# Optimization experiments

Measured on AMD Instinct MI355X. Metric: run time of the kernel, lower is better.

## Reference

```python
import jax, jax.numpy as jnp
import numpy as np

N = 20000      # nodes per snapshot
E = 160000     # edges per snapshot
T = 8          # timesteps
F_IN = 256     # nfeat
HEADS = 4      # GAT heads
C = 128        # nhid_graph (per-head GAT out, concat=False -> mean)
GH = 128       # nhid_gru
NC = 2         # nclass
NEG_SLOPE = 0.2


def setup_inputs() -> dict:
    key = jax.random.key(0)
    ks = jax.random.split(key, 16)
    s = 0.05
    return {
        "graph": jax.random.randint(ks[0], (T, 2, E), 0, N),
        "fts": jax.random.normal(ks[1], (T, N, F_IN), dtype=jnp.float32),
        "time_steps": T,
        # GATConv params (PyG-style): lin weight, att_src/att_dst, bias
        "W_gat": jax.random.normal(ks[2], (F_IN, HEADS * C), dtype=jnp.float32) * s,
        "att_src": jax.random.normal(ks[3], (HEADS, C), dtype=jnp.float32) * s,
        "att_dst": jax.random.normal(ks[4], (HEADS, C), dtype=jnp.float32) * s,
        "b_gat": jax.random.normal(ks[5], (C,), dtype=jnp.float32) * s,
        # GRU params (torch layout: [3H, in], gates order r,z,n)
        "W_ih": jax.random.normal(ks[6], (3 * GH, C), dtype=jnp.float32) * s,
        "W_hh": jax.random.normal(ks[7], (3 * GH, GH), dtype=jnp.float32) * s,
        "b_ih": jax.random.normal(ks[8], (3 * GH,), dtype=jnp.float32) * s,
        "b_hh": jax.random.normal(ks[9], (3 * GH,), dtype=jnp.float32) * s,
        # Attention ('general'): linear_in [H,H] no bias, linear_out [H,2H] no bias
        "W_att_in": jax.random.normal(ks[10], (GH, GH), dtype=jnp.float32) * s,
        "W_att_out": jax.random.normal(ks[11], (GH, 2 * GH), dtype=jnp.float32) * s,
        # final classifier
        "W_cls": jax.random.normal(ks[12], (NC, GH), dtype=jnp.float32) * s,
        "b_cls": jax.random.normal(ks[13], (NC,), dtype=jnp.float32) * s,
    }


def _segment_softmax(logits, seg, num_segments):
    # logits: [E', H], seg: [E'] destination node ids
    m = jax.ops.segment_max(logits, seg, num_segments=num_segments)
    m = jnp.where(jnp.isfinite(m), m, 0.0)
    e = jnp.exp(logits - m[seg])
    s = jax.ops.segment_sum(e, seg, num_segments=num_segments)
    return e / (s[seg] + 1e-16)


def _gat_step(x, edge_index, W_gat, att_src, att_dst, b_gat):
    # PyG GATConv: concat=False (mean over heads), negative_slope=0.2,
    # add_self_loops=True; eval mode so attention dropout is identity.
    n = x.shape[0]
    xw = (x @ W_gat).reshape(n, HEADS, C)                 # [N,H,C]
    loops = jnp.arange(n, dtype=edge_index.dtype)
    src = jnp.concatenate([edge_index[0], loops])         # [E']
    dst = jnp.concatenate([edge_index[1], loops])
    a_src = jnp.einsum('nhc,hc->nh', xw, att_src)         # [N,H]
    a_dst = jnp.einsum('nhc,hc->nh', xw, att_dst)
    alpha = jax.nn.leaky_relu(a_src[src] + a_dst[dst], NEG_SLOPE)  # [E',H]
    alpha = _segment_softmax(alpha, dst, n)
    msg = xw[src] * alpha[..., None]                      # [E',H,C]
    out = jax.ops.segment_sum(msg, dst, num_segments=n)   # [N,H,C]
    return out.mean(axis=1) + b_gat                       # [N,C]


def _gru(y, W_ih, W_hh, b_ih, b_hh):
    # y: [T, N, C]; torch GRU equations, h0 = 0
    n = y.shape[1]
    def step(h, x):
        gi = x @ W_ih.T + b_ih
        gh = h @ W_hh.T + b_hh
        i_r, i_z, i_n = jnp.split(gi, 3, axis=-1)
        h_r, h_z, h_n = jnp.split(gh, 3, axis=-1)
        r = jax.nn.sigmoid(i_r + h_r)
        z = jax.nn.sigmoid(i_z + h_z)
        nn_ = jnp.tanh(i_n + r * h_n)
        h_new = (1.0 - z) * nn_ + z * h
        return h_new, h_new
    h0 = jnp.zeros((n, GH), dtype=y.dtype)
    last, full = jax.lax.scan(step, h0, y)
    return full, last  # [T,N,GH], [N,GH]


def reference(graph, fts, time_steps, W_gat, att_src, att_dst, b_gat,
              W_ih, W_hh, b_ih, b_hh, W_att_in, W_att_out, W_cls, b_cls):
    # per-timestep GAT + leaky_relu(0.2)
    ys = [jax.nn.leaky_relu(
            _gat_step(fts[i], graph[i], W_gat, att_src, att_dst, b_gat),
            NEG_SLOPE)
          for i in range(time_steps)]
    y = jnp.stack(ys)                                     # [T,N,C]
    context, last = _gru(y, W_ih, W_hh, b_ih, b_hh)
    query = last[:, None, :]                              # [N,1,GH]
    context = jnp.transpose(context, (1, 0, 2))           # [N,T,GH]
    # Attention('general')
    q = query @ W_att_in.T                                # [N,1,GH]
    scores = jnp.einsum('nod,ntd->not', q, context)       # [N,1,T]
    w = jax.nn.softmax(scores, axis=-1)
    mix = jnp.einsum('not,ntd->nod', w, context)          # [N,1,GH]
    combined = jnp.concatenate([mix, q], axis=-1)         # [N,1,2GH]
    att_out = jnp.tanh(combined @ W_att_out.T)            # [N,1,GH]
    output = jax.nn.leaky_relu(att_out.reshape(-1, GH), NEG_SLOPE)
    logits = output @ W_cls.T + b_cls                     # [N,NC]
    return jax.nn.log_softmax(logits, axis=1)
```

## Files before the change

kernel.cpp:

```cpp
#include <hip/hip_runtime.h>
#include <hip/hip_bf16.h>
#include <math.h>

#define N_NODES 20000
#define N_EDGES 160000
#define T_STEPS 8
#define F_INC   256
#define HEADS   4
#define CCH     128
#define KC      512
#define GHD     128
#define G3      384
#define SLOPE   0.2f
#define SEG     (N_EDGES + N_NODES)

typedef unsigned short u16;
typedef __attribute__((ext_vector_type(8))) short bf16x8;
typedef __attribute__((ext_vector_type(4))) float f32x4;

__device__ __forceinline__ float leakyf(float x) { return x > 0.f ? x : SLOPE * x; }
__device__ __forceinline__ float b2f(u16 u) {
  union { unsigned int i; float f; } x; x.i = ((unsigned int)u) << 16; return x.f;
}
__device__ __forceinline__ u16 f2b(float f) {
  union { float f; unsigned int i; } u; u.f = f;
  unsigned int r = u.i + 0x7FFFu + ((u.i >> 16) & 1u);
  return (u16)(r >> 16);
}
__device__ __forceinline__ float sigf(float x) { return 1.f / (1.f + expf(-x)); }

__device__ __forceinline__ void gload16(const void* g, void* l) {
  __builtin_amdgcn_global_load_lds(
      (const __attribute__((address_space(1))) unsigned int*)g,
      (__attribute__((address_space(3))) unsigned int*)l, 16, 0, 0);
}

__device__ __forceinline__ bf16x8 cvt8(f32x4 lo, f32x4 hi) {
  union { unsigned int u[4]; bf16x8 v; } r;
  asm("v_cvt_pk_bf16_f32 %0, %1, %2" : "=v"(r.u[0]) : "v"(lo[0]), "v"(lo[1]));
  asm("v_cvt_pk_bf16_f32 %0, %1, %2" : "=v"(r.u[1]) : "v"(lo[2]), "v"(lo[3]));
  asm("v_cvt_pk_bf16_f32 %0, %1, %2" : "=v"(r.u[2]) : "v"(hi[0]), "v"(hi[1]));
  asm("v_cvt_pk_bf16_f32 %0, %1, %2" : "=v"(r.u[3]) : "v"(hi[2]), "v"(hi[3]));
  return r.v;
}

template <int OBF, int FUSE, int AFP32>
__global__ __launch_bounds__(256) void gemm_bf16(
    const void* __restrict__ Ain, const u16* __restrict__ B,
    const float* __restrict__ bias, void* __restrict__ Cout,
    int M, int K, int Nt, int swz,
    const float* __restrict__ attS, const float* __restrict__ attD,
    float* __restrict__ asrc, float* __restrict__ adst)
{
  __shared__ __align__(16) char AsRaw[128 * 32 * 4];
  __shared__ u16 Bs[128][32];
  __shared__ float s_as[128], s_ad[128];
  float* AsF = (float*)AsRaw;
  u16 (*Asb)[32] = (u16(*)[32])AsRaw;
  const int tid  = threadIdx.x;
  const int wave = tid >> 6, lane = tid & 63;
  const int wr = (wave >> 1) * 64, wc = (wave & 1) * 64;
  int bx = blockIdx.x, by = blockIdx.y;
  if (swz) {
    const int gx = gridDim.x;
    const int nwg = gx * (int)gridDim.y;
    const int lin = by * gx + bx;
    const int q = nwg >> 3, r = nwg & 7;
    const int xcd = lin & 7, idx = lin >> 3;
    const int wg = (xcd < r ? xcd * (q + 1) : r * (q + 1) + (xcd - r) * q) + idx;
    bx = wg % gx; by = wg / gx;
  }
  const int bm = by * 128, bn = bx * 128;
  const int l15 = lane & 15, g = lane >> 4;

  if (FUSE && tid < 128) { s_as[tid] = 0.f; s_ad[tid] = 0.f; }

  const int sr = tid >> 2, sd = tid & 3;
  const int ss = sd ^ ((sr >> 1) & 3);
  const u16* aS0 = 0; const u16* aS1 = 0; u16* lA0 = 0; u16* lA1 = 0;
  const float* aF[4]; float* lAF[4];
  if (AFP32) {
    const float* Af = (const float*)Ain;
    const int row0 = tid >> 3, sd8 = tid & 7;
    const int ss8 = sd8 ^ (row0 & 7);
    #pragma unroll
    for (int p = 0; p < 4; ++p) {
      int row = row0 + p * 32;
      aF[p] = Af + (size_t)min(bm + row, M - 1) * K + ss8 * 4;
      lAF[p] = AsF + (size_t)(p * 256 + (tid & ~63)) * 4;
    }
  } else {
    const u16* Ab = (const u16*)Ain;
    aS0 = Ab + (size_t)min(bm + sr,      M - 1) * K + ss * 8;
    aS1 = Ab + (size_t)min(bm + 64 + sr, M - 1) * K + ss * 8;
    lA0 = (u16*)AsRaw + (size_t)(tid & ~63) * 8;
    lA1 = lA0 + 2048;
  }
  const u16* bS0 = B + (size_t)(bn + sr)      * K + ss * 8;
  const u16* bS1 = B + (size_t)(bn + 64 + sr) * K + ss * 8;
  u16* lB0 = &Bs[0][0] + (size_t)(tid & ~63) * 8;
  u16* lB1 = lB0 + 2048;

  f32x4 acc[4][4];
  #pragma unroll
  for (int m = 0; m < 4; ++m)
    #pragma unroll
    for (int n = 0; n < 4; ++n)
      #pragma unroll
      for (int j = 0; j < 4; ++j) acc[m][n][j] = 0.f;

  const int nK = K >> 5;
  for (int kt = 0; kt < nK; ++kt) {
    const int ko = kt * 32;
    if (AFP32) {
      #pragma unroll
      for (int p = 0; p < 4; ++p) gload16(aF[p] + ko, lAF[p]);
    } else {
      gload16(aS0 + ko, lA0);
      gload16(aS1 + ko, lA1);
    }
    gload16(bS0 + ko, lB0);
    gload16(bS1 + ko, lB1);
    __syncthreads();
    bf16x8 af[4], bfr[4];
    #pragma unroll
    for (int m = 0; m < 4; ++m) {
      int row = wr + m * 16 + l15;
      if (AFP32) {
        int s0 = (2 * g) ^ (row & 7), s1 = (2 * g + 1) ^ (row & 7);
        f32x4 lo = *(const f32x4*)&AsF[row * 32 + s0 * 4];
        f32x4 hi = *(const f32x4*)&AsF[row * 32 + s1 * 4];
        af[m] = cvt8(lo, hi);
      } else {
        af[m] = *(const bf16x8*)&Asb[row][(g ^ ((row >> 1) & 3)) * 8];
      }
      int rowb = wc + m * 16 + l15;
      bfr[m] = *(const bf16x8*)&Bs[rowb][(g ^ ((rowb >> 1) & 3)) * 8];
    }
    #pragma unroll
    for (int m = 0; m < 4; ++m)
      #pragma unroll
      for (int n = 0; n < 4; ++n)
        acc[m][n] = __builtin_amdgcn_mfma_f32_16x16x32_bf16(af[m], bfr[n], acc[m][n], 0, 0, 0);
    __syncthreads();
  }
  #pragma unroll
  for (int m = 0; m < 4; ++m) {
    int row0 = bm + wr + m * 16 + g * 4;
    #pragma unroll
    for (int n = 0; n < 4; ++n) {
      int col = bn + wc + n * 16 + l15;
      float bv = bias ? bias[col] : 0.f;
      #pragma unroll
      for (int j = 0; j < 4; ++j) {
        int row = row0 + j;
        if (row < M) {
          float v = acc[m][n][j] + bv;
          if (OBF) ((u16*)Cout)[(size_t)row * Nt + col] = f2b(v);
          else     ((float*)Cout)[(size_t)row * Nt + col] = v;
        }
      }
    }
  }
  if (FUSE) {
    float ps[4][4], pd[4][4];
    #pragma unroll
    for (int m = 0; m < 4; ++m)
      #pragma unroll
      for (int j = 0; j < 4; ++j) { ps[m][j] = 0.f; pd[m][j] = 0.f; }
    #pragma unroll
    for (int n = 0; n < 4; ++n) {
      int cl = wc + n * 16 + l15;
      float wsv = attS[bn + cl], wdv = attD[bn + cl];
      #pragma unroll
      for (int m = 0; m < 4; ++m)
        #pragma unroll
        for (int j = 0; j < 4; ++j) {
          ps[m][j] = fmaf(acc[m][n][j], wsv, ps[m][j]);
          pd[m][j] = fmaf(acc[m][n][j], wdv, pd[m][j]);
        }
    }
    #pragma unroll
    for (int m = 0; m < 4; ++m)
      #pragma unroll
      for (int j = 0; j < 4; ++j)
        #pragma unroll
        for (int msk = 8; msk >= 1; msk >>= 1) {
          ps[m][j] += __shfl_xor(ps[m][j], msk);
          pd[m][j] += __shfl_xor(pd[m][j], msk);
        }
    if (l15 == 0) {
      #pragma unroll
      for (int m = 0; m < 4; ++m)
        #pragma unroll
        for (int j = 0; j < 4; ++j) {
          atomicAdd(&s_as[wr + m * 16 + g * 4 + j], ps[m][j]);
          atomicAdd(&s_ad[wr + m * 16 + g * 4 + j], pd[m][j]);
        }
    }
    __syncthreads();
    if (tid < 128) {
      int row = bm + tid;
      if (row < M) {
        int h = bn >> 7;
        asrc[(size_t)row * 4 + h] = s_as[tid];
        adst[(size_t)row * 4 + h] = s_ad[tid];
      }
    }
  }
}

__global__ void convert_weights(const float* __restrict__ w_ih, const float* __restrict__ w_hh,
                                const float* __restrict__ w_in, const float* __restrict__ w_out,
                                u16* __restrict__ wihb, u16* __restrict__ whhb,
                                u16* __restrict__ winb, u16* __restrict__ woutb)
{
  int i = blockIdx.x * 256 + threadIdx.x;
  const float* src; u16* dst; int base;
  if      (i < 6144)  { src = w_ih;  dst = wihb;  base = i; }
  else if (i < 12288) { src = w_hh;  dst = whhb;  base = i - 6144; }
  else if (i < 14336) { src = w_in;  dst = winb;  base = i - 12288; }
  else                { src = w_out; dst = woutb; base = i - 14336; }
  int o = base * 8;
  float4 v0 = *(const float4*)(src + o);
  float4 v1 = *(const float4*)(src + o + 4);
  bf16x8 ov;
  ov[0] = (short)f2b(v0.x); ov[1] = (short)f2b(v0.y);
  ov[2] = (short)f2b(v0.z); ov[3] = (short)f2b(v0.w);
  ov[4] = (short)f2b(v1.x); ov[5] = (short)f2b(v1.y);
  ov[6] = (short)f2b(v1.z); ov[7] = (short)f2b(v1.w);
  *(bf16x8*)(dst + o) = ov;
}

__global__ void conv_transpose_wgat(const float* __restrict__ src, u16* __restrict__ dst) {
  int idx = blockIdx.x * 256 + threadIdx.x;
  if (idx >= KC * F_INC) return;
  int n = idx >> 8, k = idx & 255;
  dst[(size_t)n * F_INC + k] = f2b(src[(size_t)k * KC + n]);
}

__global__ void count_kernel(const int* __restrict__ graph, int* __restrict__ counts) {
  int e = blockIdx.x * 256 + threadIdx.x;
  int t = blockIdx.y;
  if (e < N_EDGES) {
    int d = graph[(size_t)t * 2 * N_EDGES + N_EDGES + e];
    atomicAdd(&counts[t * N_NODES + d], 1);
  }
}

__global__ __launch_bounds__(1024) void scan_kernel(
    const int* __restrict__ counts, int* __restrict__ offs)
{
  const int t = blockIdx.x;
  const int tid = threadIdx.x, lane = tid & 63, w = tid >> 6;
  __shared__ int s_wt[16];
  int carry = 0;
  const int base_abs = t * SEG;
  for (int base = 0; base < N_NODES; base += 1024) {
    int i = base + tid;
    int v = (i < N_NODES) ? (counts[t * N_NODES + i] + 1) : 0;
    int x = v;
    #pragma unroll
    for (int d = 1; d < 64; d <<= 1) {
      int nvl = __shfl_up(x, d, 64);
      if (lane >= d) x += nvl;
    }
    if (lane == 63) s_wt[w] = x;
    __syncthreads();
    if (tid < 16) {
      int y = s_wt[tid];
      #pragma unroll
      for (int d = 1; d < 16; d <<= 1) {
        int nvl = __shfl_up(y, d, 64);
        if (tid >= d) y += nvl;
      }
      s_wt[tid] = y;
    }
    __syncthreads();
    int wbase = (w > 0) ? s_wt[w - 1] : 0;
    int total = s_wt[15];
    if (i < N_NODES) offs[t * (N_NODES + 1) + i] = base_abs + carry + wbase + x - v;
    carry += total;
    __syncthreads();
  }
  if (tid == 0) offs[t * (N_NODES + 1) + N_NODES] = base_abs + carry;
}

__global__ void scatter_kernel(const int* __restrict__ graph, const int* __restrict__ offs,
                               int* __restrict__ cursor, int* __restrict__ ssrc)
{
  int i = blockIdx.x * 256 + threadIdx.x;
  int t = blockIdx.y;
  if (i >= SEG) return;
  int s, d;
  if (i < N_EDGES) {
    s = graph[(size_t)t * 2 * N_EDGES + i];
    d = graph[(size_t)t * 2 * N_EDGES + N_EDGES + i];
  } else {
    s = d = i - N_EDGES;
  }
  int pos = offs[t * (N_NODES + 1) + d] + atomicAdd(&cursor[t * N_NODES + d], 1);
  ssrc[pos] = s;
}

__global__ __launch_bounds__(256) void aggregate_kernel(
    const u16* __restrict__ xw, const float* __restrict__ a_src,
    const float* __restrict__ a_dst, const float* __restrict__ b_gat,
    const int* __restrict__ offs, const int* __restrict__ ssrc,
    u16* __restrict__ yout)
{
  const int wv = threadIdx.x >> 6, lane = threadIdx.x & 63;
  const int nd = blockIdx.x * 4 + wv;
  const int t  = blockIdx.y;
  const int ob = t * (N_NODES + 1) + nd;
  const int beg = offs[ob], end = offs[ob + 1];
  const size_t rowbase = (size_t)t * N_NODES;
  const int he   = lane & 3;
  const int eidx = lane >> 2;
  const int hl   = lane >> 4;
  const float advh = a_dst[(rowbase + nd) * 4 + he];

  float m = -INFINITY, ssum = 0.f;
  float acc[8] = {0.f,0.f,0.f,0.f,0.f,0.f,0.f,0.f};

#define FMA8(W, X)                                                        \
    { float _w = (W);                                                     \
      acc[0] = fmaf(_w, __uint_as_float((unsigned)(X).x << 16), acc[0]);  \
      acc[1] = fmaf(_w, __uint_as_float((unsigned)(X).x & 0xffff0000u), acc[1]); \
      acc[2] = fmaf(_w, __uint_as_float((unsigned)(X).y << 16), acc[2]);  \
      acc[3] = fmaf(_w, __uint_as_float((unsigned)(X).y & 0xffff0000u), acc[3]); \
      acc[4] = fmaf(_w, __uint_as_float((unsigned)(X).z << 16), acc[4]);  \
      acc[5] = fmaf(_w, __uint_as_float((unsigned)(X).z & 0xffff0000u), acc[5]); \
      acc[6] = fmaf(_w, __uint_as_float((unsigned)(X).w << 16), acc[6]);  \
      acc[7] = fmaf(_w, __uint_as_float((unsigned)(X).w & 0xffff0000u), acc[7]); }
#define LDE(SVAR) (*(const int4*)&xw[(rowbase + (SVAR)) * KC + lane * 8])

  for (int base = beg; base < end; base += 16) {
    const int cnt = min(16, end - base);
    const int e = base + eidx;
    const int sidx = (e < end) ? ssrc[e] : ssrc[base];
    const float av = a_src[(rowbase + sidx) * 4 + he];
    const float a = (eidx < cnt) ? leakyf(av + advh) : -INFINITY;
    float cm = a;
    cm = fmaxf(cm, __shfl_xor(cm, 4));
    cm = fmaxf(cm, __shfl_xor(cm, 8));
    cm = fmaxf(cm, __shfl_xor(cm, 16));
    cm = fmaxf(cm, __shfl_xor(cm, 32));
    const float nm = fmaxf(m, cm);
    const float sc = expf(m - nm);
    const float w = expf(a - nm);
    float ts = w;
    ts += __shfl_xor(ts, 4);
    ts += __shfl_xor(ts, 8);
    ts += __shfl_xor(ts, 16);
    ts += __shfl_xor(ts, 32);
    ssum = ssum * sc + ts;
    m = nm;
    const float schl = __shfl(sc, hl);
    #pragma unroll
    for (int k = 0; k < 8; ++k) acc[k] *= schl;

    const int cpad = (cnt + 3) & ~3;
    int b4 = 0;
    for (; b4 + 8 <= cpad; b4 += 8) {
      const int s0 = __shfl(sidx, (b4 + 0) << 2);
      const int s1 = __shfl(sidx, (b4 + 1) << 2);
      const int s2 = __shfl(sidx, (b4 + 2) << 2);
      const int s3 = __shfl(sidx, (b4 + 3) << 2);
      const int s4 = __shfl(sidx, (b4 + 4) << 2);
      const int s5 = __shfl(sidx, (b4 + 5) << 2);
      const int s6 = __shfl(sidx, (b4 + 6) << 2);
      const int s7 = __shfl(sidx, (b4 + 7) << 2);
      const int4 x0 = LDE(s0); const int4 x1 = LDE(s1);
      const int4 x2 = LDE(s2); const int4 x3 = LDE(s3);
      const int4 x4 = LDE(s4); const int4 x5 = LDE(s5);
      const int4 x6 = LDE(s6); const int4 x7 = LDE(s7);
      const float w0 = __shfl(w, ((b4 + 0) << 2) + hl);
      const float w1 = __shfl(w, ((b4 + 1) << 2) + hl);
      const float w2 = __shfl(w, ((b4 + 2) << 2) + hl);
      const float w3 = __shfl(w, ((b4 + 3) << 2) + hl);
      const float w4 = __shfl(w, ((b4 + 4) << 2) + hl);
      const float w5 = __shfl(w, ((b4 + 5) << 2) + hl);
      const float w6 = __shfl(w, ((b4 + 6) << 2) + hl);
      const float w7 = __shfl(w, ((b4 + 7) << 2) + hl);
      FMA8(w0, x0); FMA8(w1, x1); FMA8(w2, x2); FMA8(w3, x3);
      FMA8(w4, x4); FMA8(w5, x5); FMA8(w6, x6); FMA8(w7, x7);
    }
    if (b4 < cpad) {
      const int s0 = __shfl(sidx, (b4 + 0) << 2);
      const int s1 = __shfl(sidx, (b4 + 1) << 2);
      const int s2 = __shfl(sidx, (b4 + 2) << 2);
      const int s3 = __shfl(sidx, (b4 + 3) << 2);
      const int4 x0 = LDE(s0); const int4 x1 = LDE(s1);
      const int4 x2 = LDE(s2); const int4 x3 = LDE(s3);
      const float w0 = __shfl(w, ((b4 + 0) << 2) + hl);
      const float w1 = __shfl(w, ((b4 + 1) << 2) + hl);
      const float w2 = __shfl(w, ((b4 + 2) << 2) + hl);
      const float w3 = __shfl(w, ((b4 + 3) << 2) + hl);
      FMA8(w0, x0); FMA8(w1, x1); FMA8(w2, x2); FMA8(w3, x3);
    }
  }
#undef LDE
#undef FMA8

  const float sh = __shfl(ssum, hl);
  const float inv = 1.f / (sh + 1e-16f);
  #pragma unroll
  for (int k = 0; k < 8; ++k) {
    acc[k] *= inv;
    acc[k] += __shfl_xor(acc[k], 16);
    acc[k] += __shfl_xor(acc[k], 32);
  }
  if (lane < 16) {
    bf16x8 ov;
    #pragma unroll
    for (int k = 0; k < 8; ++k) {
      float v = acc[k] * 0.25f + b_gat[lane * 8 + k];
      ov[k] = (short)f2b(leakyf(v));
    }
    *(bf16x8*)&yout[(rowbase + nd) * GHD + lane * 8] = ov;
  }
}

__global__ __launch_bounds__(256) void gru_seq(
    const u16* __restrict__ Whh, const float* __restrict__ b_hh,
    const u16* __restrict__ giall, u16* __restrict__ ctx)
{
  __shared__ u16 hA[32][128];
  __shared__ u16 reg2[12288];
  u16 (*Bs)[32] = (u16(*)[32])reg2;
  const int tid = threadIdx.x, lane = tid & 63, wv = tid >> 6;
  const int l15 = lane & 15, g = lane >> 4;
  const int bm = blockIdx.x * 32;

  const int sr = tid >> 2, sd = tid & 3;
  const int ssb = sd ^ ((sr >> 1) & 3);
  const u16* bS[6]; u16* lB[6];
  #pragma unroll
  for (int p = 0; p < 6; ++p) {
    bS[p] = Whh + (size_t)(sr + p * 64) * GHD + ssb * 8;
    lB[p] = reg2 + (size_t)(p * 256 + (tid & ~63)) * 8;
  }
  float bbv[6];
  #pragma unroll
  for (int n = 0; n < 6; ++n) bbv[n] = b_hh[wv * 96 + n * 16 + l15];

  const int cr = tid >> 3;
  const int cg = (tid & 7) * 8;
  const int grow = bm + cr;
  const size_t gb = (size_t)grow * G3;
  const size_t cb = (size_t)grow * GHD;
  float hp[2][8];

  #pragma unroll
  for (int q = 0; q < 2; ++q) {
    const int c0 = cg + q * 64;
    bf16x8 ir8 = *(const bf16x8*)&giall[gb + c0];
    bf16x8 iz8 = *(const bf16x8*)&giall[gb + 128 + c0];
    bf16x8 in8 = *(const bf16x8*)&giall[gb + 256 + c0];
    float4 br0 = *(const float4*)&b_hh[c0];       float4 br1 = *(const float4*)&b_hh[c0 + 4];
    float4 bz0 = *(const float4*)&b_hh[128 + c0]; float4 bz1 = *(const float4*)&b_hh[128 + c0 + 4];
    float4 bn0 = *(const float4*)&b_hh[256 + c0]; float4 bn1 = *(const float4*)&b_hh[256 + c0 + 4];
    float bhr[8] = {br0.x, br0.y, br0.z, br0.w, br1.x, br1.y, br1.z, br1.w};
    float bhz[8] = {bz0.x, bz0.y, bz0.z, bz0.w, bz1.x, bz1.y, bz1.z, bz1.w};
    float bhn[8] = {bn0.x, bn0.y, bn0.z, bn0.w, bn1.x, bn1.y, bn1.z, bn1.w};
    bf16x8 hv;
    #pragma unroll
    for (int k = 0; k < 8; ++k) {
      float rr = sigf(b2f((u16)ir8[k]) + bhr[k]);
      float zz = sigf(b2f((u16)iz8[k]) + bhz[k]);
      float nn = tanhf(b2f((u16)in8[k]) + rr * bhn[k]);
      float h = (1.f - zz) * nn;
      hp[q][k] = h;
      hv[k] = (short)f2b(h);
    }
    const int sl = (c0 >> 3) ^ (cr & 7);
    *(bf16x8*)&hA[cr][sl * 8] = hv;
    *(bf16x8*)&ctx[cb + c0] = hv;
  }
  __syncthreads();

  for (int t = 1; t < T_STEPS; ++t) {
    const u16* gi_t = giall + (size_t)t * N_NODES * G3;
    u16* ctx_t = ctx + (size_t)t * N_NODES * GHD;
    f32x4 acc[2][6];
    #pragma unroll
    for (int m = 0; m < 2; ++m)
      #pragma unroll
      for (int n = 0; n < 6; ++n)
        #pragma unroll
        for (int j = 0; j < 4; ++j) acc[m][n][j] = 0.f;

    #pragma unroll
    for (int kt = 0; kt < 4; ++kt) {
      const int ko = kt * 32;
      #pragma unroll
      for (int p = 0; p < 6; ++p) gload16(bS[p] + ko, lB[p]);
      __syncthreads();
      bf16x8 af[2], bfr[6];
      #pragma unroll
      for (int m = 0; m < 2; ++m) {
        int row = m * 16 + l15;
        int sl = (kt * 4 + g) ^ (row & 7);
        af[m] = *(const bf16x8*)&hA[row][sl * 8];
      }
      #pragma unroll
      for (int n = 0; n < 6; ++n) {
        int rowb = wv * 96 + n * 16 + l15;
        bfr[n] = *(const bf16x8*)&Bs[rowb][(g ^ ((rowb >> 1) & 3)) * 8];
      }
      #pragma unroll
      for (int m = 0; m < 2; ++m)
        #pragma unroll
        for (int n = 0; n < 6; ++n)
          acc[m][n] = __builtin_amdgcn_mfma_f32_16x16x32_bf16(af[m], bfr[n], acc[m][n], 0, 0, 0);
      __syncthreads();
    }
    #pragma unroll
    for (int m = 0; m < 2; ++m)
      #pragma unroll
      for (int n = 0; n < 6; ++n) {
        int c = wv * 96 + n * 16 + l15;
        #pragma unroll
        for (int j = 0; j < 4; ++j) {
          int r = m * 16 + g * 4 + j;
          reg2[r * 384 + (((c >> 3) ^ (r & 7)) << 3) + (c & 7)] = f2b(acc[m][n][j] + bbv[n]);
        }
      }
    __syncthreads();
    #pragma unroll
    for (int q = 0; q < 2; ++q) {
      const int c0 = cg + q * 64;
      const int sl0 = ((c0 >> 3) ^ (cr & 7));
      const int sl1 = (((128 + c0) >> 3) ^ (cr & 7));
      const int sl2 = (((256 + c0) >> 3) ^ (cr & 7));
      bf16x8 hr8 = *(bf16x8*)&reg2[cr * 384 + sl0 * 8];
      bf16x8 hz8 = *(bf16x8*)&reg2[cr * 384 + sl1 * 8];
      bf16x8 hn8 = *(bf16x8*)&reg2[cr * 384 + sl2 * 8];
      bf16x8 ir8 = *(const bf16x8*)&gi_t[gb + c0];
      bf16x8 iz8 = *(const bf16x8*)&gi_t[gb + 128 + c0];
      bf16x8 in8 = *(const bf16x8*)&gi_t[gb + 256 + c0];
      bf16x8 hv;
      #pragma unroll
      for (int k = 0; k < 8; ++k) {
        float rr = sigf(b2f((u16)ir8[k]) + b2f((u16)hr8[k]));
        float zz = sigf(b2f((u16)iz8[k]) + b2f((u16)hz8[k]));
        float nn = tanhf(b2f((u16)in8[k]) + rr * b2f((u16)hn8[k]));
        float h = (1.f - zz) * nn + zz * hp[q][k];
        hp[q][k] = h;
        hv[k] = (short)f2b(h);
      }
      const int slh = (c0 >> 3) ^ (cr & 7);
      *(bf16x8*)&hA[cr][slh * 8] = hv;
      *(bf16x8*)&ctx_t[cb + c0] = hv;
    }
    __syncthreads();
  }
}

__global__ __launch_bounds__(256) void attn_mid(
    const u16* __restrict__ ctx, const float* __restrict__ q,
    u16* __restrict__ comb)
{
  const int node = blockIdx.x * 4 + (threadIdx.x >> 6);
  const int lane = threadIdx.x & 63;
  if (node >= N_NODES) return;
  const float q0 = q[(size_t)node * GHD + lane];
  const float q1 = q[(size_t)node * GHD + 64 + lane];
  float c0[T_STEPS], c1[T_STEPS], w[T_STEPS];
  float mx = -1e30f;
  #pragma unroll
  for (int t = 0; t < T_STEPS; ++t) {
    const u16* cr = ctx + ((size_t)t * N_NODES + node) * GHD;
    c0[t] = b2f(cr[lane]); c1[t] = b2f(cr[64 + lane]);
    float p = q0 * c0[t] + q1 * c1[t];
    #pragma unroll
    for (int m = 32; m >= 1; m >>= 1) p += __shfl_xor(p, m);
    w[t] = p;
    mx = fmaxf(mx, p);
  }
  float s = 0.f;
  #pragma unroll
  for (int t = 0; t < T_STEPS; ++t) { w[t] = expf(w[t] - mx); s += w[t]; }
  const float inv = 1.f / s;
  float m0 = 0.f, m1 = 0.f;
  #pragma unroll
  for (int t = 0; t < T_STEPS; ++t) { m0 = fmaf(w[t], c0[t], m0); m1 = fmaf(w[t], c1[t], m1); }
  m0 *= inv; m1 *= inv;
  u16* cb = comb + (size_t)node * 2 * GHD;
  cb[lane]       = f2b(m0);
  cb[64 + lane]  = f2b(m1);
  cb[128 + lane] = f2b(q0);
  cb[192 + lane] = f2b(q1);
}

__global__ __launch_bounds__(256) void logits_kernel(
    const u16* __restrict__ ao, const float* __restrict__ W_cls,
    const float* __restrict__ b_cls, float* __restrict__ out)
{
  const int node = blockIdx.x * 4 + (threadIdx.x >> 6);
  const int lane = threadIdx.x & 63;
  if (node >= N_NODES) return;
  float o0 = leakyf(tanhf(b2f(ao[(size_t)node * GHD + lane])));
  float o1 = leakyf(tanhf(b2f(ao[(size_t)node * GHD + 64 + lane])));
  float p0 = o0 * W_cls[lane] + o1 * W_cls[64 + lane];
  float p1 = o0 * W_cls[128 + lane] + o1 * W_cls[192 + lane];
  #pragma unroll
  for (int m = 32; m >= 1; m >>= 1) { p0 += __shfl_xor(p0, m); p1 += __shfl_xor(p1, m); }
  if (lane == 0) {
    float l0 = p0 + b_cls[0];
    float l1 = p1 + b_cls[1];
    float mx = fmaxf(l0, l1);
    float lse = mx + logf(expf(l0 - mx) + expf(l1 - mx));
    out[(size_t)node * 2 + 0] = l0 - lse;
    out[(size_t)node * 2 + 1] = l1 - lse;
  }
}

extern "C" void kernel_launch(void* const* d_in, const int* in_sizes, int n_in,
                              void* d_out, int out_size, void* d_ws, size_t ws_size,
                              hipStream_t stream)
{
  const int*   graph     = (const int*)  d_in[0];
  const float* fts       = (const float*)d_in[1];
  const float* W_gat     = (const float*)d_in[3];
  const float* att_src   = (const float*)d_in[4];
  const float* att_dst   = (const float*)d_in[5];
  const float* b_gat     = (const float*)d_in[6];
  const float* W_ih      = (const float*)d_in[7];
  const float* W_hh      = (const float*)d_in[8];
  const float* b_ih      = (const float*)d_in[9];
  const float* b_hh      = (const float*)d_in[10];
  const float* W_att_in  = (const float*)d_in[11];
  const float* W_att_out = (const float*)d_in[12];
  const float* W_cls     = (const float*)d_in[13];
  const float* b_cls     = (const float*)d_in[14];
  float* out = (float*)d_out;

  char* ws = (char*)d_ws;
  size_t off = 0;
  auto alloc = [&](size_t bytes) {
    void* p = ws + off;
    off = (off + bytes + 255) & ~(size_t)255;
    return p;
  };
  const size_t NT = (size_t)T_STEPS * N_NODES;
  u16*   wgatT = (u16*)alloc((size_t)KC * F_INC * 2);
  u16*   wihb  = (u16*)alloc((size_t)G3 * GHD * 2);
  u16*   whhb  = (u16*)alloc((size_t)G3 * GHD * 2);
  u16*   winb  = (u16*)alloc((size_t)GHD * GHD * 2);
  u16*   woutb = (u16*)alloc((size_t)GHD * 2 * GHD * 2);
  u16*   xw    = (u16*)alloc(NT * KC * 2);
  float* asrc  = (float*)alloc(NT * 4 * 4);
  float* adst  = (float*)alloc(NT * 4 * 4);
  u16*   yall  = (u16*)alloc(NT * GHD * 2);
  u16*   giall = (u16*)alloc(NT * G3 * 2);
  u16*   ctx   = (u16*)alloc(NT * GHD * 2);
  float* qf    = (float*)alloc((size_t)N_NODES * GHD * 4);
  u16*   comb  = (u16*)alloc((size_t)N_NODES * 2 * GHD * 2);
  u16*   aob   = (u16*)alloc((size_t)N_NODES * GHD * 2);
  int* counts  = (int*)alloc((size_t)2 * T_STEPS * N_NODES * 4);
  int* cursor  = counts + T_STEPS * N_NODES;
  int* offs    = (int*)alloc((size_t)T_STEPS * (N_NODES + 1) * 4);
  int* ssrc    = (int*)alloc((size_t)T_STEPS * SEG * 4);

  conv_transpose_wgat<<<dim3((KC * F_INC + 255) / 256), 256, 0, stream>>>(W_gat, wgatT);
  convert_weights<<<dim3(72), 256, 0, stream>>>(W_ih, W_hh, W_att_in, W_att_out,
                                                wihb, whhb, winb, woutb);

  hipMemsetAsync(counts, 0, (size_t)2 * T_STEPS * N_NODES * 4, stream);
  count_kernel<<<dim3(N_EDGES / 256, T_STEPS), 256, 0, stream>>>(graph, counts);
  scan_kernel<<<dim3(T_STEPS), 1024, 0, stream>>>(counts, offs);
  scatter_kernel<<<dim3((SEG + 255) / 256, T_STEPS), 256, 0, stream>>>(graph, offs, cursor, ssrc);

  gemm_bf16<1, 1, 1><<<dim3(KC / 128, (int)(NT / 128)), 256, 0, stream>>>(
      fts, wgatT, nullptr, xw, (int)NT, F_INC, KC, 1, att_src, att_dst, asrc, adst);

  aggregate_kernel<<<dim3(N_NODES / 4, T_STEPS), 256, 0, stream>>>(
      xw, asrc, adst, b_gat, offs, ssrc, yall);

  gemm_bf16<1, 0, 0><<<dim3(G3 / 128, (int)(NT / 128)), 256, 0, stream>>>(
      yall, wihb, b_ih, giall, (int)NT, GHD, G3, 1, nullptr, nullptr, nullptr, nullptr);

  gru_seq<<<dim3(N_NODES / 32), 256, 0, stream>>>(whhb, b_hh, giall, ctx);

  gemm_bf16<0, 0, 0><<<dim3(1, (N_NODES + 127) / 128), 256, 0, stream>>>(
      ctx + (size_t)(T_STEPS - 1) * N_NODES * GHD, winb, nullptr, qf,
      N_NODES, GHD, GHD, 0, nullptr, nullptr, nullptr, nullptr);
  attn_mid<<<dim3(N_NODES / 4), 256, 0, stream>>>(ctx, qf, comb);
  gemm_bf16<1, 0, 0><<<dim3(1, (N_NODES + 127) / 128), 256, 0, stream>>>(
      comb, woutb, nullptr, aob, N_NODES, 2 * GHD, GHD, 0, nullptr, nullptr, nullptr, nullptr);
  logits_kernel<<<dim3(N_NODES / 4), 256, 0, stream>>>(aob, W_cls, b_cls, out);
}
```

Before: 744.4 us.

## Fuse classifier and log-softmax into attention output GEMM; parallelize CSR offset scan

Adds a FUSE==2 epilogue mode to the bf16 GEMM that applies tanh and leaky_relu to the attention-output accumulators, projects them onto the two classifier rows, and writes the log-softmax directly. This drops the intermediate attention-output buffer and the separate logits kernel. The per-timestep single-block scan, which ran only 8 blocks, becomes a three-phase global scan across all timesteps so many blocks can work on it. The offsets array becomes one flat prefix sum, which the scatter and aggregate indexing now rely on.

```diff
diff --git a/kernel.cpp b/kernel.cpp
--- a/kernel.cpp
+++ b/kernel.cpp
@@ -13,6 +13,8 @@
 #define G3      384
 #define SLOPE   0.2f
 #define SEG     (N_EDGES + N_NODES)
+#define TN      (T_STEPS * N_NODES)
+#define SCAN_BLKS ((TN + 1023) / 1024)
 
 typedef unsigned short u16;
 typedef __attribute__((ext_vector_type(8))) short bf16x8;
@@ -144,20 +146,22 @@
         acc[m][n] = __builtin_amdgcn_mfma_f32_16x16x32_bf16(af[m], bfr[n], acc[m][n], 0, 0, 0);
     __syncthreads();
   }
-  #pragma unroll
-  for (int m = 0; m < 4; ++m) {
-    int row0 = bm + wr + m * 16 + g * 4;
-    #pragma unroll
-    for (int n = 0; n < 4; ++n) {
-      int col = bn + wc + n * 16 + l15;
-      float bv = bias ? bias[col] : 0.f;
-      #pragma unroll
-      for (int j = 0; j < 4; ++j) {
-        int row = row0 + j;
-        if (row < M) {
-          float v = acc[m][n][j] + bv;
-          if (OBF) ((u16*)Cout)[(size_t)row * Nt + col] = f2b(v);
-          else     ((float*)Cout)[(size_t)row * Nt + col] = v;
+  if (FUSE != 2) {
+    #pragma unroll
+    for (int m = 0; m < 4; ++m) {
+      int row0 = bm + wr + m * 16 + g * 4;
+      #pragma unroll
+      for (int n = 0; n < 4; ++n) {
+        int col = bn + wc + n * 16 + l15;
+        float bv = bias ? bias[col] : 0.f;
+        #pragma unroll
+        for (int j = 0; j < 4; ++j) {
+          int row = row0 + j;
+          if (row < M) {
+            float v = acc[m][n][j] + bv;
+            if (OBF) ((u16*)Cout)[(size_t)row * Nt + col] = f2b(v);
+            else     ((float*)Cout)[(size_t)row * Nt + col] = v;
+          }
         }
       }
     }
@@ -176,8 +180,10 @@
       for (int m = 0; m < 4; ++m)
         #pragma unroll
         for (int j = 0; j < 4; ++j) {
-          ps[m][j] = fmaf(acc[m][n][j], wsv, ps[m][j]);
-          pd[m][j] = fmaf(acc[m][n][j], wdv, pd[m][j]);
+          float av = acc[m][n][j];
+          if (FUSE == 2) av = leakyf(tanhf(av));
+          ps[m][j] = fmaf(av, wsv, ps[m][j]);
+          pd[m][j] = fmaf(av, wdv, pd[m][j]);
         }
     }
     #pragma unroll
@@ -202,9 +208,18 @@
     if (tid < 128) {
       int row = bm + tid;
       if (row < M) {
-        int h = bn >> 7;
-        asrc[(size_t)row * 4 + h] = s_as[tid];
-        adst[(size_t)row * 4 + h] = s_ad[tid];
+        if (FUSE == 1) {
+          int h = bn >> 7;
+          asrc[(size_t)row * 4 + h] = s_as[tid];
+          adst[(size_t)row * 4 + h] = s_ad[tid];
+        } else {
+          float l0 = s_as[tid] + bias[0];
+          float l1 = s_ad[tid] + bias[1];
+          float mx = fmaxf(l0, l1);
+          float lse = mx + logf(expf(l0 - mx) + expf(l1 - mx));
+          asrc[(size_t)row * 2 + 0] = l0 - lse;
+          asrc[(size_t)row * 2 + 1] = l1 - lse;
+        }
       }
     }
   }
@@ -248,42 +263,57 @@
   }
 }
 
-__global__ __launch_bounds__(1024) void scan_kernel(
-    const int* __restrict__ counts, int* __restrict__ offs)
+__global__ __launch_bounds__(1024) void scanA(
+    const int* __restrict__ counts, int* __restrict__ offs, int* __restrict__ bsums)
 {
-  const int t = blockIdx.x;
   const int tid = threadIdx.x, lane = tid & 63, w = tid >> 6;
   __shared__ int s_wt[16];
+  int i = blockIdx.x * 1024 + tid;
+  int v = (i < TN) ? (counts[i] + 1) : 0;
+  int x = v;
+  #pragma unroll
+  for (int d = 1; d < 64; d <<= 1) {
+    int nvl = __shfl_up(x, d, 64);
+    if (lane >= d) x += nvl;
+  }
+  if (lane == 63) s_wt[w] = x;
+  __syncthreads();
+  if (tid < 16) {
+    int y = s_wt[tid];
+    #pragma unroll
+    for (int d = 1; d < 16; d <<= 1) {
+      int nvl = __shfl_up(y, d, 64);
+      if (tid >= d) y += nvl;
+    }
+    s_wt[tid] = y;
+  }
+  __syncthreads();
+  int wbase = (w > 0) ? s_wt[w - 1] : 0;
+  if (i < TN) offs[i] = wbase + x - v;
+  if (tid == 1023) bsums[blockIdx.x] = s_wt[15];
+}
+
+__global__ void scanB(int* __restrict__ bsums, int* __restrict__ offs) {
+  const int lane = threadIdx.x;
   int carry = 0;
-  const int base_abs = t * SEG;
-  for (int base = 0; base < N_NODES; base += 1024) {
-    int i = base + tid;
-    int v = (i < N_NODES) ? (counts[t * N_NODES + i] + 1) : 0;
+  for (int base = 0; base < 192; base += 64) {
+    int idx = base + lane;
+    int v = (idx < SCAN_BLKS) ? bsums[idx] : 0;
     int x = v;
     #pragma unroll
     for (int d = 1; d < 64; d <<= 1) {
       int nvl = __shfl_up(x, d, 64);
       if (lane >= d) x += nvl;
     }
-    if (lane == 63) s_wt[w] = x;
-    __syncthreads();
-    if (tid < 16) {
-      int y = s_wt[tid];
-      #pragma unroll
-      for (int d = 1; d < 16; d <<= 1) {
-        int nvl = __shfl_up(y, d, 64);
-        if (tid >= d) y += nvl;
-      }
-      s_wt[tid] = y;
-    }
-    __syncthreads();
-    int wbase = (w > 0) ? s_wt[w - 1] : 0;
-    int total = s_wt[15];
-    if (i < N_NODES) offs[t * (N_NODES + 1) + i] = base_abs + carry + wbase + x - v;
-    carry += total;
-    __syncthreads();
-  }
-  if (tid == 0) offs[t * (N_NODES + 1) + N_NODES] = base_abs + carry;
+    if (idx < SCAN_BLKS) bsums[idx] = carry + x - v;
+    carry += __shfl(x, 63);
+  }
+  if (lane == 0) offs[TN] = carry;
+}
+
+__global__ __launch_bounds__(1024) void scanC(int* __restrict__ offs, const int* __restrict__ bsums) {
+  int i = blockIdx.x * 1024 + threadIdx.x;
+  if (i < TN) offs[i] += bsums[blockIdx.x];
 }
 
 __global__ void scatter_kernel(const int* __restrict__ graph, const int* __restrict__ offs,
@@ -299,7 +329,7 @@
   } else {
     s = d = i - N_EDGES;
   }
-  int pos = offs[t * (N_NODES + 1) + d] + atomicAdd(&cursor[t * N_NODES + d], 1);
+  int pos = offs[t * N_NODES + d] + atomicAdd(&cursor[t * N_NODES + d], 1);
   ssrc[pos] = s;
 }
 
@@ -312,7 +342,7 @@
   const int wv = threadIdx.x >> 6, lane = threadIdx.x & 63;
   const int nd = blockIdx.x * 4 + wv;
   const int t  = blockIdx.y;
-  const int ob = t * (N_NODES + 1) + nd;
+  const int ob = t * N_NODES + nd;
   const int beg = offs[ob], end = offs[ob + 1];
   const size_t rowbase = (size_t)t * N_NODES;
   const int he   = lane & 3;
@@ -594,29 +624,6 @@
   cb[192 + lane] = f2b(q1);
 }
 
-__global__ __launch_bounds__(256) void logits_kernel(
-    const u16* __restrict__ ao, const float* __restrict__ W_cls,
-    const float* __restrict__ b_cls, float* __restrict__ out)
-{
-  const int node = blockIdx.x * 4 + (threadIdx.x >> 6);
-  const int lane = threadIdx.x & 63;
-  if (node >= N_NODES) return;
-  float o0 = leakyf(tanhf(b2f(ao[(size_t)node * GHD + lane])));
-  float o1 = leakyf(tanhf(b2f(ao[(size_t)node * GHD + 64 + lane])));
-  float p0 = o0 * W_cls[lane] + o1 * W_cls[64 + lane];
-  float p1 = o0 * W_cls[128 + lane] + o1 * W_cls[192 + lane];
-  #pragma unroll
-  for (int m = 32; m >= 1; m >>= 1) { p0 += __shfl_xor(p0, m); p1 += __shfl_xor(p1, m); }
-  if (lane == 0) {
-    float l0 = p0 + b_cls[0];
-    float l1 = p1 + b_cls[1];
-    float mx = fmaxf(l0, l1);
-    float lse = mx + logf(expf(l0 - mx) + expf(l1 - mx));
-    out[(size_t)node * 2 + 0] = l0 - lse;
-    out[(size_t)node * 2 + 1] = l1 - lse;
-  }
-}
-
 extern "C" void kernel_launch(void* const* d_in, const int* in_sizes, int n_in,
                               void* d_out, int out_size, void* d_ws, size_t ws_size,
                               hipStream_t stream)
@@ -644,7 +651,7 @@
     off = (off + bytes + 255) & ~(size_t)255;
     return p;
   };
-  const size_t NT = (size_t)T_STEPS * N_NODES;
+  const size_t NT = (size_t)TN;
   u16*   wgatT = (u16*)alloc((size_t)KC * F_INC * 2);
   u16*   wihb  = (u16*)alloc((size_t)G3 * GHD * 2);
   u16*   whhb  = (u16*)alloc((size_t)G3 * GHD * 2);
@@ -658,19 +665,21 @@
   u16*   ctx   = (u16*)alloc(NT * GHD * 2);
   float* qf    = (float*)alloc((size_t)N_NODES * GHD * 4);
   u16*   comb  = (u16*)alloc((size_t)N_NODES * 2 * GHD * 2);
-  u16*   aob   = (u16*)alloc((size_t)N_NODES * GHD * 2);
-  int* counts  = (int*)alloc((size_t)2 * T_STEPS * N_NODES * 4);
-  int* cursor  = counts + T_STEPS * N_NODES;
-  int* offs    = (int*)alloc((size_t)T_STEPS * (N_NODES + 1) * 4);
+  int* counts  = (int*)alloc((size_t)2 * TN * 4);
+  int* cursor  = counts + TN;
+  int* offs    = (int*)alloc((size_t)(TN + 1) * 4);
+  int* bsums   = (int*)alloc((size_t)256 * 4);
   int* ssrc    = (int*)alloc((size_t)T_STEPS * SEG * 4);
 
   conv_transpose_wgat<<<dim3((KC * F_INC + 255) / 256), 256, 0, stream>>>(W_gat, wgatT);
   convert_weights<<<dim3(72), 256, 0, stream>>>(W_ih, W_hh, W_att_in, W_att_out,
                                                 wihb, whhb, winb, woutb);
 
-  hipMemsetAsync(counts, 0, (size_t)2 * T_STEPS * N_NODES * 4, stream);
+  hipMemsetAsync(counts, 0, (size_t)2 * TN * 4, stream);
   count_kernel<<<dim3(N_EDGES / 256, T_STEPS), 256, 0, stream>>>(graph, counts);
-  scan_kernel<<<dim3(T_STEPS), 1024, 0, stream>>>(counts, offs);
+  scanA<<<dim3(SCAN_BLKS), 1024, 0, stream>>>(counts, offs, bsums);
+  scanB<<<dim3(1), 64, 0, stream>>>(bsums, offs);
+  scanC<<<dim3(SCAN_BLKS), 1024, 0, stream>>>(offs, bsums);
   scatter_kernel<<<dim3((SEG + 255) / 256, T_STEPS), 256, 0, stream>>>(graph, offs, cursor, ssrc);
 
   gemm_bf16<1, 1, 1><<<dim3(KC / 128, (int)(NT / 128)), 256, 0, stream>>>(
@@ -688,7 +697,7 @@
       ctx + (size_t)(T_STEPS - 1) * N_NODES * GHD, winb, nullptr, qf,
       N_NODES, GHD, GHD, 0, nullptr, nullptr, nullptr, nullptr);
   attn_mid<<<dim3(N_NODES / 4), 256, 0, stream>>>(ctx, qf, comb);
-  gemm_bf16<1, 0, 0><<<dim3(1, (N_NODES + 127) / 128), 256, 0, stream>>>(
-      comb, woutb, nullptr, aob, N_NODES, 2 * GHD, GHD, 0, nullptr, nullptr, nullptr, nullptr);
-  logits_kernel<<<dim3(N_NODES / 4), 256, 0, stream>>>(aob, W_cls, b_cls, out);
-}
+  gemm_bf16<0, 2, 0><<<dim3(1, (N_NODES + 127) / 128), 256, 0, stream>>>(
+      comb, woutb, b_cls, nullptr, N_NODES, 2 * GHD, GHD, 0,
+      W_cls, W_cls + GHD, out, nullptr);
+}
```

Result: faster. 724.6 us (-2.7%).
